# Kernel tuning notes

Hardware: AMD Instinct MI355X
Metric: run time of the kernel (lower is better)

The kernel has to match this reference:

```python
import jax, jax.numpy as jnp
import numpy as np

N = 50000      # nodes
E = 600000     # edges
D = 128        # inp_dim == emb_dim
R = 100        # num_rels
B = 4          # num_bases
L = 2          # num_layers
EPS = 1e-5


def setup_inputs() -> dict:
    key = jax.random.key(0)
    ks = jax.random.split(key, 4 + 6 * L)
    inp = {
        "feat": jax.random.normal(ks[0], (N, D), dtype=jnp.float32),
        "src": jax.random.randint(ks[1], (E,), 0, N),
        "dst": jax.random.randint(ks[2], (E,), 0, N),
        "etype": jax.random.randint(ks[3], (E,), 0, R),
    }
    for l in range(L):
        o = 4 + 6 * l
        s = 1.0 / np.sqrt(D)
        inp[f"V{l}"] = jax.random.normal(ks[o + 0], (B, D, D), dtype=jnp.float32) * s
        inp[f"comb{l}"] = jax.random.normal(ks[o + 1], (R, B), dtype=jnp.float32)
        inp[f"loop{l}"] = jax.random.normal(ks[o + 2], (D, D), dtype=jnp.float32) * s
        inp[f"bias{l}"] = jax.random.normal(ks[o + 3], (D,), dtype=jnp.float32) * 0.01
        inp[f"gamma{l}"] = jnp.ones((D,), dtype=jnp.float32)
        inp[f"beta{l}"] = jnp.zeros((D,), dtype=jnp.float32)
    return inp


def _rel_graph_conv(x, src, dst, etype, V, comb, W_loop, bias):
    # basis-decomposed relational conv: W_r = sum_b comb[r,b] * V[b]
    xb = jnp.einsum('nd,bdo->nbo', x, V)            # [N, B, D] project onto bases once
    msg = jnp.einsum('ebo,eb->eo', xb[src], comb[etype])  # [E, D] per-edge typed message
    agg = jax.ops.segment_sum(msg, dst, num_segments=N)   # scatter-add to destinations
    h = agg + x @ W_loop + bias                     # self-loop + bias (DGL defaults)
    return jax.nn.relu(h)


def _batch_norm(h, gamma, beta):
    mu = jnp.mean(h, axis=0)
    var = jnp.mean(jnp.square(h - mu), axis=0)      # biased var (training-mode BN)
    return gamma * (h - mu) * jax.lax.rsqrt(var + EPS) + beta


def reference(feat, src, dst, etype,
              V0, comb0, loop0, bias0, gamma0, beta0,
              V1, comb1, loop1, bias1, gamma1, beta1):
    h = feat
    h = _rel_graph_conv(h, src, dst, etype, V0, comb0, loop0, bias0)
    h = _batch_norm(h, gamma0, beta0)
    h = _rel_graph_conv(h, src, dst, etype, V1, comb1, loop1, bias1)
    h = _batch_norm(h, gamma1, beta1)
    return h  # JK='last'
```

## Files before the change

### kernel.cpp

```cpp
#include <hip/hip_runtime.h>
#include <hip/hip_bf16.h>

#define Nn 50000
#define Ee 600000
#define Dd 128
#define EPSc 1e-5f
#define GX 391
#define NB 196

typedef unsigned int u32;
typedef unsigned short u16;
typedef short s16x8 __attribute__((ext_vector_type(8)));
typedef float f32x4 __attribute__((ext_vector_type(4)));

__device__ inline float bf2f(u32 lo16) { return __uint_as_float(lo16 << 16); }
__device__ inline u16 f2bf(float f) {
    u32 b = __float_as_uint(f);
    return (u16)((b + 0x7fffu + ((b >> 16) & 1u)) >> 16);
}
__device__ inline void gload16(const void* g, void* l) {
    __builtin_amdgcn_global_load_lds(
        (const __attribute__((address_space(1))) u32*)g,
        (__attribute__((address_space(3))) u32*)l, 16, 0, 0);
}

__global__ __launch_bounds__(256) void hist_k(const int* __restrict__ dst,
                                              int* __restrict__ cnt) {
    int e = blockIdx.x * 256 + threadIdx.x;
    if (e < Ee) atomicAdd(&cnt[dst[e]], 1);
}

__global__ __launch_bounds__(256) void scanA_k(const int* __restrict__ cnt,
                                               int* __restrict__ rowp,
                                               int* __restrict__ bsum) {
    __shared__ int ws4[4];
    const int tid = threadIdx.x, lane = tid & 63, w = tid >> 6;
    const int i = blockIdx.x * 256 + tid;
    int v = (i < Nn) ? cnt[i] : 0;
    int incl = v;
#pragma unroll
    for (int off = 1; off < 64; off <<= 1) {
        int u = __shfl_up(incl, off, 64);
        if (lane >= off) incl += u;
    }
    if (lane == 63) ws4[w] = incl;
    __syncthreads();
    if (tid == 0) {
        int run = 0;
#pragma unroll
        for (int j = 0; j < 4; j++) { int s = ws4[j]; ws4[j] = run; run += s; }
    }
    __syncthreads();
    incl += ws4[w];
    if (i < Nn) rowp[i + 1] = incl;
    if (tid == 255) bsum[blockIdx.x] = incl;
}

__global__ __launch_bounds__(256) void scanB_k(const int* __restrict__ bsum,
                                               int* __restrict__ boff) {
    __shared__ int ws4[4];
    const int tid = threadIdx.x, lane = tid & 63, w = tid >> 6;
    int v = (tid < NB) ? bsum[tid] : 0;
    int incl = v;
#pragma unroll
    for (int off = 1; off < 64; off <<= 1) {
        int u = __shfl_up(incl, off, 64);
        if (lane >= off) incl += u;
    }
    if (lane == 63) ws4[w] = incl;
    __syncthreads();
    if (tid == 0) {
        int run = 0;
#pragma unroll
        for (int j = 0; j < 4; j++) { int s = ws4[j]; ws4[j] = run; run += s; }
    }
    __syncthreads();
    if (tid < NB) boff[tid] = incl + ws4[w] - v;
}

__global__ __launch_bounds__(256) void scanC_k(const int* __restrict__ boff,
                                               int* __restrict__ rowp,
                                               int* __restrict__ cursor) {
    const int i = blockIdx.x * 256 + threadIdx.x;
    if (i < Nn) {
        int v = rowp[i + 1] + boff[blockIdx.x];
        rowp[i + 1] = v;
        if (i + 1 < Nn) cursor[i + 1] = v;
    }
    if (i == 0) { rowp[0] = 0; cursor[0] = 0; }
}

__global__ __launch_bounds__(256) void scatter_k(const int* __restrict__ src,
                                                 const int* __restrict__ dst,
                                                 const int* __restrict__ et,
                                                 int* __restrict__ cursor,
                                                 int2* __restrict__ se) {
    int e = blockIdx.x * 256 + threadIdx.x;
    if (e < Ee) {
        int pos = atomicAdd(&cursor[dst[e]], 1);
        se[pos] = make_int2(src[e], et[e]);
    }
}

__global__ __launch_bounds__(256) void conv_k(const float* __restrict__ in,
                                              u16* __restrict__ out) {
    const int total = Nn * 32;
    for (int i = blockIdx.x * 256 + threadIdx.x; i < total; i += gridDim.x * 256) {
        float4 v = ((const float4*)in)[i];
        ((ushort4*)out)[i] = make_ushort4(f2bf(v.x), f2bf(v.y), f2bf(v.z), f2bf(v.w));
    }
}

__global__ __launch_bounds__(256) void wprep2_k(const float* __restrict__ V0,
                                                const float* __restrict__ loop0,
                                                const float* __restrict__ V1,
                                                const float* __restrict__ loop1,
                                                u16* __restrict__ Wt) {
    int i = blockIdx.x * 256 + threadIdx.x;
    if (i >= 2 * 128 * 640) return;
    int l = i / 81920, r = i - l * 81920;
    int c = r / 640, k = r - c * 640;
    const float* V = l ? V1 : V0;
    const float* lp = l ? loop1 : loop0;
    float v = (k < 512) ? V[(size_t)k * 128 + c] : lp[(size_t)(k - 512) * 128 + c];
    Wt[i] = f2bf(v);
}

__global__ __launch_bounds__(256) void agg_k(const u16* __restrict__ x16,
                                             const int2* __restrict__ se,
                                             const int* __restrict__ rowp,
                                             const float* __restrict__ comb,
                                             u16* __restrict__ yb16) {
    const int wv = threadIdx.x >> 6;
    const int lane = threadIdx.x & 63;
    const int nA = blockIdx.x * 8 + wv * 2;
    const int begA = rowp[nA], endA = rowp[nA + 1], endB = rowp[nA + 2];
    const int begB = endA;
    const int eLA = endA - 1, eLB = endB - 1;
    const u32 co = (u32)lane * 2u;

    float A0x = 0.f, A0y = 0.f, A1x = 0.f, A1y = 0.f;
    float A2x = 0.f, A2y = 0.f, A3x = 0.f, A3y = 0.f;
    float B0x = 0.f, B0y = 0.f, B1x = 0.f, B1y = 0.f;
    float B2x = 0.f, B2y = 0.f, B3x = 0.f, B3y = 0.f;

    const int degA = endA - begA, degB = endB - begB;
    const int nst = (max(degA, degB) + 3) >> 2;

    for (int s = 0; s < nst; s++) {
        const int eA = begA + s * 4, eB = begB + s * 4;
        const int mA = endA - eA, mB = endB - eB;
        int2 rc[8];
        u32 xv[8];
#pragma unroll
        for (int j = 0; j < 4; j++) {
            rc[j]     = se[(mA > 0) ? min(eA + j, eLA) : 0];
            rc[4 + j] = se[(mB > 0) ? min(eB + j, eLB) : 0];
        }
#pragma unroll
        for (int j = 0; j < 8; j++)
            xv[j] = *(const u32*)&x16[(size_t)(u32)rc[j].x * 128 + co];
#pragma unroll
        for (int j = 0; j < 4; j++) {
            if (j >= mA) xv[j] = 0;
            if (j >= mB) xv[4 + j] = 0;
        }
#pragma unroll
        for (int j = 0; j < 4; j++) {
            {
                const float4 c = ((const float4*)comb)[rc[j].y];
                const float fx = bf2f(xv[j] & 0xffffu);
                const float fy = bf2f(xv[j] >> 16);
                A0x += c.x * fx; A0y += c.x * fy;
                A1x += c.y * fx; A1y += c.y * fy;
                A2x += c.z * fx; A2y += c.z * fy;
                A3x += c.w * fx; A3y += c.w * fy;
            }
            {
                const float4 c = ((const float4*)comb)[rc[4 + j].y];
                const float fx = bf2f(xv[4 + j] & 0xffffu);
                const float fy = bf2f(xv[4 + j] >> 16);
                B0x += c.x * fx; B0y += c.x * fy;
                B1x += c.y * fx; B1y += c.y * fy;
                B2x += c.z * fx; B2y += c.z * fy;
                B3x += c.w * fx; B3y += c.w * fy;
            }
        }
    }
    u32* ypA = (u32*)(yb16 + (size_t)nA * 512);
    ypA[lane]       = (u32)f2bf(A0x) | ((u32)f2bf(A0y) << 16);
    ypA[64 + lane]  = (u32)f2bf(A1x) | ((u32)f2bf(A1y) << 16);
    ypA[128 + lane] = (u32)f2bf(A2x) | ((u32)f2bf(A2y) << 16);
    ypA[192 + lane] = (u32)f2bf(A3x) | ((u32)f2bf(A3y) << 16);
    u32* ypB = ypA + 256;
    ypB[lane]       = (u32)f2bf(B0x) | ((u32)f2bf(B0y) << 16);
    ypB[64 + lane]  = (u32)f2bf(B1x) | ((u32)f2bf(B1y) << 16);
    ypB[128 + lane] = (u32)f2bf(B2x) | ((u32)f2bf(B2y) << 16);
    ypB[192 + lane] = (u32)f2bf(B3x) | ((u32)f2bf(B3y) << 16);
}

__global__ __launch_bounds__(256) void gemm_mfma_k(const u16* __restrict__ yb16,
                                                   const u16* __restrict__ x16,
                                                   const u16* __restrict__ Wt,
                                                   const float* __restrict__ bias,
                                                   float* __restrict__ OUT,
                                                   float* __restrict__ partials) {
    __shared__ __align__(16) char As[8192];
    __shared__ __align__(16) char Bs[8192];
    const int tid = threadIdx.x;
    const int lane = tid & 63, wid = tid >> 6;
    const int wr = wid >> 1, wc = wid & 1;
    const int bm = blockIdx.x * 128;

    f32x4 acc[4][4] = {};

    const int r0 = wid * 32;
    const int lrow = lane >> 2;
    const int sphys = lane & 3;
    const int rowL0 = r0 + lrow, rowL1 = r0 + 16 + lrow;
    const int slog0 = (sphys ^ ((rowL0 >> 1) & 3)) * 8;
    const int slog1 = (sphys ^ ((rowL1 >> 1) & 3)) * 8;
    int ga0 = bm + rowL0; if (ga0 >= Nn) ga0 = Nn - 1;
    int ga1 = bm + rowL1; if (ga1 >= Nn) ga1 = Nn - 1;

    for (int k0 = 0; k0 < 640; k0 += 32) {
        __syncthreads();
        const u16 *as0, *as1;
        if (k0 < 512) {
            as0 = yb16 + (size_t)ga0 * 512 + k0 + slog0;
            as1 = yb16 + (size_t)ga1 * 512 + k0 + slog1;
        } else {
            as0 = x16 + (size_t)ga0 * 128 + (k0 - 512) + slog0;
            as1 = x16 + (size_t)ga1 * 128 + (k0 - 512) + slog1;
        }
        gload16(as0, &As[r0 * 64]);
        gload16(as1, &As[(r0 + 16) * 64]);
        gload16(Wt + (size_t)rowL0 * 640 + k0 + slog0, &Bs[r0 * 64]);
        gload16(Wt + (size_t)rowL1 * 640 + k0 + slog1, &Bs[(r0 + 16) * 64]);
        __syncthreads();
        s16x8 a[4], b[4];
#pragma unroll
        for (int m = 0; m < 4; m++) {
            int row = wr * 64 + m * 16 + (lane & 15);
            a[m] = *(const s16x8*)&As[row * 64 + (((lane >> 4) ^ ((row >> 1) & 3)) << 4)];
            int col = wc * 64 + m * 16 + (lane & 15);
            b[m] = *(const s16x8*)&Bs[col * 64 + (((lane >> 4) ^ ((col >> 1) & 3)) << 4)];
        }
#pragma unroll
        for (int m = 0; m < 4; m++)
#pragma unroll
            for (int n = 0; n < 4; n++)
                acc[m][n] = __builtin_amdgcn_mfma_f32_16x16x32_bf16(a[m], b[n],
                                                                    acc[m][n], 0, 0, 0);
    }
    float bv[4], cs[4] = {}, cq[4] = {};
#pragma unroll
    for (int n = 0; n < 4; n++) bv[n] = bias[wc * 64 + n * 16 + (lane & 15)];
#pragma unroll
    for (int m = 0; m < 4; m++) {
        const int rb = bm + wr * 64 + m * 16 + ((lane >> 4) << 2);
#pragma unroll
        for (int e = 0; e < 4; e++) {
            const int r = rb + e;
            if (r < Nn) {
                float* op = OUT + (size_t)r * 128 + wc * 64 + (lane & 15);
#pragma unroll
                for (int n = 0; n < 4; n++) {
                    float v = fmaxf(acc[m][n][e] + bv[n], 0.f);
                    op[n * 16] = v;
                    cs[n] += v;
                    cq[n] += v * v;
                }
            }
        }
    }
#pragma unroll
    for (int n = 0; n < 4; n++) {
        cs[n] += __shfl_xor(cs[n], 16);
        cs[n] += __shfl_xor(cs[n], 32);
        cq[n] += __shfl_xor(cq[n], 16);
        cq[n] += __shfl_xor(cq[n], 32);
    }
    __syncthreads();
    float* red = (float*)As;
    if (wr == 1 && lane < 16) {
#pragma unroll
        for (int n = 0; n < 4; n++) {
            const int col = wc * 64 + n * 16 + lane;
            red[col] = cs[n];
            red[128 + col] = cq[n];
        }
    }
    __syncthreads();
    if (wr == 0 && lane < 16) {
        float* pp = partials + (size_t)blockIdx.x * 256;
#pragma unroll
        for (int n = 0; n < 4; n++) {
            const int col = wc * 64 + n * 16 + lane;
            pp[col] = cs[n] + red[col];
            pp[128 + col] = cq[n] + red[128 + col];
        }
    }
}

__global__ __launch_bounds__(256) void red_k(const float* __restrict__ partials,
                                             float* __restrict__ stats) {
    const int c = threadIdx.x;
    float s0 = 0.f, s1 = 0.f, s2 = 0.f, s3 = 0.f;
    int b = 0;
    for (; b + 4 <= GX; b += 4) {
        s0 += partials[(size_t)(b + 0) * 256 + c];
        s1 += partials[(size_t)(b + 1) * 256 + c];
        s2 += partials[(size_t)(b + 2) * 256 + c];
        s3 += partials[(size_t)(b + 3) * 256 + c];
    }
    for (; b < GX; b++) s0 += partials[(size_t)b * 256 + c];
    stats[c] = (s0 + s1) + (s2 + s3);
}

__global__ __launch_bounds__(256) void norm_k(const float* __restrict__ h,
                                              const float* __restrict__ stats,
                                              const float* __restrict__ gamma,
                                              const float* __restrict__ beta,
                                              float* __restrict__ outp,
                                              u16* __restrict__ xb) {
    const float invN = 1.0f / (float)Nn;
    int total = Nn * 32;
    for (int i = blockIdx.x * blockDim.x + threadIdx.x; i < total;
         i += gridDim.x * blockDim.x) {
        int c = (i & 31) * 4;
        float4 v = ((const float4*)h)[i];
        float4 o;
        {
            float mu = stats[c + 0] * invN;
            float var = stats[Dd + c + 0] * invN - mu * mu;
            o.x = gamma[c + 0] * (v.x - mu) * rsqrtf(var + EPSc) + beta[c + 0];
        }
        {
            float mu = stats[c + 1] * invN;
            float var = stats[Dd + c + 1] * invN - mu * mu;
            o.y = gamma[c + 1] * (v.y - mu) * rsqrtf(var + EPSc) + beta[c + 1];
        }
        {
            float mu = stats[c + 2] * invN;
            float var = stats[Dd + c + 2] * invN - mu * mu;
            o.z = gamma[c + 2] * (v.z - mu) * rsqrtf(var + EPSc) + beta[c + 2];
        }
        {
            float mu = stats[c + 3] * invN;
            float var = stats[Dd + c + 3] * invN - mu * mu;
            o.w = gamma[c + 3] * (v.w - mu) * rsqrtf(var + EPSc) + beta[c + 3];
        }
        if (outp) ((float4*)outp)[i] = o;
        if (xb) ((ushort4*)xb)[i] = make_ushort4(f2bf(o.x), f2bf(o.y),
                                                 f2bf(o.z), f2bf(o.w));
    }
}

extern "C" void kernel_launch(void* const* d_in, const int* in_sizes, int n_in,
                              void* d_out, int out_size, void* d_ws, size_t ws_size,
                              hipStream_t stream) {
    const float* feat = (const float*)d_in[0];
    const int* src = (const int*)d_in[1];
    const int* dst = (const int*)d_in[2];
    const int* et = (const int*)d_in[3];
    float* out = (float*)d_out;

    char* p = (char*)d_ws;
    u16* yb16 = (u16*)p;     p += (size_t)Nn * 512 * 2;
    u16* x16 = (u16*)p;      p += (size_t)Nn * 128 * 2;
    u16* Wt = (u16*)p;       p += (size_t)2 * 128 * 640 * 2;
    int* rowp = (int*)p;     p += ((((size_t)(Nn + 1) * 4) + 15) & ~15ull);
    int2* se = (int2*)p;     p += (size_t)Ee * 8;
    float* partials = (float*)p;  p += (size_t)GX * 256 * 4;
    float* stats = (float*)p;     p += 2 * Dd * 4;
    int* bsum = (int*)p;          p += ((NB * 4 + 15) & ~15);
    int* boff = (int*)p;          p += ((NB * 4 + 15) & ~15);
    int* cursor = (int*)yb16;

    hipMemsetAsync(cursor, 0, (size_t)Nn * 4, stream);
    hist_k<<<(Ee + 255) / 256, 256, 0, stream>>>(dst, cursor);
    scanA_k<<<NB, 256, 0, stream>>>(cursor, rowp, bsum);
    scanB_k<<<1, 256, 0, stream>>>(bsum, boff);
    scanC_k<<<NB, 256, 0, stream>>>(boff, rowp, cursor);
    scatter_k<<<(Ee + 255) / 256, 256, 0, stream>>>(src, dst, et, cursor, se);
    conv_k<<<1024, 256, 0, stream>>>(feat, x16);
    wprep2_k<<<(2 * 128 * 640 + 255) / 256, 256, 0, stream>>>(
        (const float*)d_in[4], (const float*)d_in[6],
        (const float*)d_in[10], (const float*)d_in[12], Wt);

    for (int l = 0; l < 2; l++) {
        const float* comb = (const float*)d_in[4 + 6 * l + 1];
        const float* bias = (const float*)d_in[4 + 6 * l + 3];
        const float* gamma = (const float*)d_in[4 + 6 * l + 4];
        const float* beta = (const float*)d_in[4 + 6 * l + 5];

        agg_k<<<Nn / 8, 256, 0, stream>>>(x16, se, rowp, comb, yb16);
        gemm_mfma_k<<<GX, 256, 0, stream>>>(yb16, x16, Wt + (size_t)l * 81920,
                                            bias, out, partials);
        red_k<<<1, 256, 0, stream>>>(partials, stats);
        norm_k<<<2048, 256, 0, stream>>>(out, stats, gamma, beta,
                                         (l == 0) ? nullptr : out,
                                         (l == 0) ? x16 : nullptr);
    }
}
```

Measured before the change: 281.9 us.

## Store pre-norm activations as bf16 and simplify aggregation to one node per wave

The GEMM epilogue now writes the ReLU output as bf16 into a new workspace buffer instead of fp32 into the output, and the normalization kernel reads it back as bf16. This halves the intermediate write and read traffic between GEMM and BN, though the final output loses some precision before normalization. The aggregation kernel also drops the two-nodes-per-wave interleaving in favour of one node per wave with a four-edge unrolled loop, which doubles the grid and reduces register pressure but gives each wave less memory-level parallelism.

```diff
diff --git a/kernel.cpp b/kernel.cpp
--- a/kernel.cpp
+++ b/kernel.cpp
@@ -131,79 +131,58 @@
                                              const int* __restrict__ rowp,
                                              const float* __restrict__ comb,
                                              u16* __restrict__ yb16) {
-    const int wv = threadIdx.x >> 6;
+    const int node = blockIdx.x * 4 + (threadIdx.x >> 6);
     const int lane = threadIdx.x & 63;
-    const int nA = blockIdx.x * 8 + wv * 2;
-    const int begA = rowp[nA], endA = rowp[nA + 1], endB = rowp[nA + 2];
-    const int begB = endA;
-    const int eLA = endA - 1, eLB = endB - 1;
-    const u32 co = (u32)lane * 2u;
-
-    float A0x = 0.f, A0y = 0.f, A1x = 0.f, A1y = 0.f;
-    float A2x = 0.f, A2y = 0.f, A3x = 0.f, A3y = 0.f;
-    float B0x = 0.f, B0y = 0.f, B1x = 0.f, B1y = 0.f;
-    float B2x = 0.f, B2y = 0.f, B3x = 0.f, B3y = 0.f;
-
-    const int degA = endA - begA, degB = endB - begB;
-    const int nst = (max(degA, degB) + 3) >> 2;
-
-    for (int s = 0; s < nst; s++) {
-        const int eA = begA + s * 4, eB = begB + s * 4;
-        const int mA = endA - eA, mB = endB - eB;
-        int2 rc[8];
-        u32 xv[8];
-#pragma unroll
-        for (int j = 0; j < 4; j++) {
-            rc[j]     = se[(mA > 0) ? min(eA + j, eLA) : 0];
-            rc[4 + j] = se[(mB > 0) ? min(eB + j, eLB) : 0];
-        }
-#pragma unroll
-        for (int j = 0; j < 8; j++)
-            xv[j] = *(const u32*)&x16[(size_t)(u32)rc[j].x * 128 + co];
-#pragma unroll
-        for (int j = 0; j < 4; j++) {
-            if (j >= mA) xv[j] = 0;
-            if (j >= mB) xv[4 + j] = 0;
-        }
-#pragma unroll
-        for (int j = 0; j < 4; j++) {
-            {
-                const float4 c = ((const float4*)comb)[rc[j].y];
-                const float fx = bf2f(xv[j] & 0xffffu);
-                const float fy = bf2f(xv[j] >> 16);
-                A0x += c.x * fx; A0y += c.x * fy;
-                A1x += c.y * fx; A1y += c.y * fy;
-                A2x += c.z * fx; A2y += c.z * fy;
-                A3x += c.w * fx; A3y += c.w * fy;
-            }
-            {
-                const float4 c = ((const float4*)comb)[rc[4 + j].y];
-                const float fx = bf2f(xv[4 + j] & 0xffffu);
-                const float fy = bf2f(xv[4 + j] >> 16);
-                B0x += c.x * fx; B0y += c.x * fy;
-                B1x += c.y * fx; B1y += c.y * fy;
-                B2x += c.z * fx; B2y += c.z * fy;
-                B3x += c.w * fx; B3y += c.w * fy;
-            }
-        }
-    }
-    u32* ypA = (u32*)(yb16 + (size_t)nA * 512);
-    ypA[lane]       = (u32)f2bf(A0x) | ((u32)f2bf(A0y) << 16);
-    ypA[64 + lane]  = (u32)f2bf(A1x) | ((u32)f2bf(A1y) << 16);
-    ypA[128 + lane] = (u32)f2bf(A2x) | ((u32)f2bf(A2y) << 16);
-    ypA[192 + lane] = (u32)f2bf(A3x) | ((u32)f2bf(A3y) << 16);
-    u32* ypB = ypA + 256;
-    ypB[lane]       = (u32)f2bf(B0x) | ((u32)f2bf(B0y) << 16);
-    ypB[64 + lane]  = (u32)f2bf(B1x) | ((u32)f2bf(B1y) << 16);
-    ypB[128 + lane] = (u32)f2bf(B2x) | ((u32)f2bf(B2y) << 16);
-    ypB[192 + lane] = (u32)f2bf(B3x) | ((u32)f2bf(B3y) << 16);
+    const int beg = rowp[node], end = rowp[node + 1];
+    float a0x = 0.f, a0y = 0.f, a1x = 0.f, a1y = 0.f;
+    float a2x = 0.f, a2y = 0.f, a3x = 0.f, a3y = 0.f;
+    const int eL = end - 1;
+    const int co = lane * 2;
+
+    for (int e0 = beg; e0 < end; e0 += 4) {
+        const int m = end - e0;
+        const int2 rc0 = se[e0];
+        const int2 rc1 = se[min(e0 + 1, eL)];
+        const int2 rc2 = se[min(e0 + 2, eL)];
+        const int2 rc3 = se[min(e0 + 3, eL)];
+        u32 x0 = *(const u32*)&x16[(size_t)rc0.x * 128 + co];
+        u32 x1 = *(const u32*)&x16[(size_t)rc1.x * 128 + co];
+        u32 x2 = *(const u32*)&x16[(size_t)rc2.x * 128 + co];
+        u32 x3 = *(const u32*)&x16[(size_t)rc3.x * 128 + co];
+        if (m < 4) x3 = 0;
+        if (m < 3) x2 = 0;
+        if (m < 2) x1 = 0;
+        const float4 c0 = ((const float4*)comb)[rc0.y];
+        const float4 c1 = ((const float4*)comb)[rc1.y];
+        const float4 c2 = ((const float4*)comb)[rc2.y];
+        const float4 c3 = ((const float4*)comb)[rc3.y];
+#define ACC1(c, xv)                                        \
+        {                                                  \
+            const float fx = bf2f((xv) & 0xffffu);         \
+            const float fy = bf2f((xv) >> 16);             \
+            a0x += c.x * fx; a0y += c.x * fy;              \
+            a1x += c.y * fx; a1y += c.y * fy;              \
+            a2x += c.z * fx; a2y += c.z * fy;              \
+            a3x += c.w * fx; a3y += c.w * fy;              \
+        }
+        ACC1(c0, x0)
+        ACC1(c1, x1)
+        ACC1(c2, x2)
+        ACC1(c3, x3)
+#undef ACC1
+    }
+    u32* yp = (u32*)(yb16 + (size_t)node * 512);
+    yp[lane]       = (u32)f2bf(a0x) | ((u32)f2bf(a0y) << 16);
+    yp[64 + lane]  = (u32)f2bf(a1x) | ((u32)f2bf(a1y) << 16);
+    yp[128 + lane] = (u32)f2bf(a2x) | ((u32)f2bf(a2y) << 16);
+    yp[192 + lane] = (u32)f2bf(a3x) | ((u32)f2bf(a3y) << 16);
 }
 
 __global__ __launch_bounds__(256) void gemm_mfma_k(const u16* __restrict__ yb16,
                                                    const u16* __restrict__ x16,
                                                    const u16* __restrict__ Wt,
                                                    const float* __restrict__ bias,
-                                                   float* __restrict__ OUT,
+                                                   u16* __restrict__ H16,
                                                    float* __restrict__ partials) {
     __shared__ __align__(16) char As[8192];
     __shared__ __align__(16) char Bs[8192];
@@ -263,11 +242,11 @@
         for (int e = 0; e < 4; e++) {
             const int r = rb + e;
             if (r < Nn) {
-                float* op = OUT + (size_t)r * 128 + wc * 64 + (lane & 15);
+                u16* hp = H16 + (size_t)r * 128 + wc * 64 + (lane & 15);
 #pragma unroll
                 for (int n = 0; n < 4; n++) {
                     float v = fmaxf(acc[m][n][e] + bv[n], 0.f);
-                    op[n * 16] = v;
+                    hp[n * 16] = f2bf(v);
                     cs[n] += v;
                     cq[n] += v * v;
                 }
@@ -318,7 +297,7 @@
     stats[c] = (s0 + s1) + (s2 + s3);
 }
 
-__global__ __launch_bounds__(256) void norm_k(const float* __restrict__ h,
+__global__ __launch_bounds__(256) void norm_k(const u16* __restrict__ h16,
                                               const float* __restrict__ stats,
                                               const float* __restrict__ gamma,
                                               const float* __restrict__ beta,
@@ -329,27 +308,27 @@
     for (int i = blockIdx.x * blockDim.x + threadIdx.x; i < total;
          i += gridDim.x * blockDim.x) {
         int c = (i & 31) * 4;
-        float4 v = ((const float4*)h)[i];
+        ushort4 hv = ((const ushort4*)h16)[i];
         float4 o;
         {
             float mu = stats[c + 0] * invN;
             float var = stats[Dd + c + 0] * invN - mu * mu;
-            o.x = gamma[c + 0] * (v.x - mu) * rsqrtf(var + EPSc) + beta[c + 0];
+            o.x = gamma[c + 0] * (bf2f(hv.x) - mu) * rsqrtf(var + EPSc) + beta[c + 0];
         }
         {
             float mu = stats[c + 1] * invN;
             float var = stats[Dd + c + 1] * invN - mu * mu;
-            o.y = gamma[c + 1] * (v.y - mu) * rsqrtf(var + EPSc) + beta[c + 1];
+            o.y = gamma[c + 1] * (bf2f(hv.y) - mu) * rsqrtf(var + EPSc) + beta[c + 1];
         }
         {
             float mu = stats[c + 2] * invN;
             float var = stats[Dd + c + 2] * invN - mu * mu;
-            o.z = gamma[c + 2] * (v.z - mu) * rsqrtf(var + EPSc) + beta[c + 2];
+            o.z = gamma[c + 2] * (bf2f(hv.z) - mu) * rsqrtf(var + EPSc) + beta[c + 2];
         }
         {
             float mu = stats[c + 3] * invN;
             float var = stats[Dd + c + 3] * invN - mu * mu;
-            o.w = gamma[c + 3] * (v.w - mu) * rsqrtf(var + EPSc) + beta[c + 3];
+            o.w = gamma[c + 3] * (bf2f(hv.w) - mu) * rsqrtf(var + EPSc) + beta[c + 3];
         }
         if (outp) ((float4*)outp)[i] = o;
         if (xb) ((ushort4*)xb)[i] = make_ushort4(f2bf(o.x), f2bf(o.y),
@@ -369,6 +348,7 @@
     char* p = (char*)d_ws;
     u16* yb16 = (u16*)p;     p += (size_t)Nn * 512 * 2;
     u16* x16 = (u16*)p;      p += (size_t)Nn * 128 * 2;
+    u16* h16 = (u16*)p;      p += (size_t)Nn * 128 * 2;
     u16* Wt = (u16*)p;       p += (size_t)2 * 128 * 640 * 2;
     int* rowp = (int*)p;     p += ((((size_t)(Nn + 1) * 4) + 15) & ~15ull);
     int2* se = (int2*)p;     p += (size_t)Ee * 8;
@@ -395,11 +375,11 @@
         const float* gamma = (const float*)d_in[4 + 6 * l + 4];
         const float* beta = (const float*)d_in[4 + 6 * l + 5];
 
-        agg_k<<<Nn / 8, 256, 0, stream>>>(x16, se, rowp, comb, yb16);
+        agg_k<<<Nn / 4, 256, 0, stream>>>(x16, se, rowp, comb, yb16);
         gemm_mfma_k<<<GX, 256, 0, stream>>>(yb16, x16, Wt + (size_t)l * 81920,
-                                            bias, out, partials);
+                                            bias, h16, partials);
         red_k<<<1, 256, 0, stream>>>(partials, stats);
-        norm_k<<<2048, 256, 0, stream>>>(out, stats, gamma, beta,
+        norm_k<<<2048, 256, 0, stream>>>(h16, stats, gamma, beta,
                                          (l == 0) ? nullptr : out,
                                          (l == 0) ? x16 : nullptr);
     }
```

Measured after the change: 267.6 us. 1.05x faster.
